# Optimization experiments

Measured on AMD Instinct MI355X. Metric: run time of the kernel, lower is better.

## Reference

```python
import jax, jax.numpy as jnp
import numpy as np

D_MODEL = 2560
NUM_HEADS = 32
NUM_KV_HEADS = 8
HEAD_DIM = 128
ROPE_THETA = 5e6
EPS = 1e-6
G = NUM_KV_HEADS
Q_PER_KV = NUM_HEADS // NUM_KV_HEADS


def setup_inputs() -> dict:
    key = jax.random.key(0)
    ks = jax.random.split(key, 5)
    B, S = 1, 2048
    scale = 0.02
    return {
        "x": jax.random.normal(ks[0], (B, S, D_MODEL), jnp.float32),
        "Wq": jax.random.normal(ks[1], (NUM_HEADS * HEAD_DIM, D_MODEL), jnp.float32) * scale,
        "Wk": jax.random.normal(ks[2], (NUM_KV_HEADS * HEAD_DIM, D_MODEL), jnp.float32) * scale,
        "Wv": jax.random.normal(ks[3], (NUM_KV_HEADS * HEAD_DIM, D_MODEL), jnp.float32) * scale,
        "Wo": jax.random.normal(ks[4], (D_MODEL, NUM_HEADS * HEAD_DIM), jnp.float32) * scale,
        "q_norm_w": jnp.ones((HEAD_DIM,), jnp.float32),
        "k_norm_w": jnp.ones((HEAD_DIM,), jnp.float32),
    }


def _rms_norm(x, w):
    var = jnp.mean(jnp.square(x), axis=-1, keepdims=True)
    return x * jax.lax.rsqrt(var + EPS) * w


def _rope(x, pos):
    # x: (b, h, s, d); HF-style rotate_half RoPE
    d = x.shape[-1]
    inv_freq = 1.0 / (ROPE_THETA ** (jnp.arange(0, d, 2, dtype=jnp.float32) / d))
    ang = pos[:, None].astype(jnp.float32) * inv_freq[None, :]      # (s, d/2)
    cos = jnp.concatenate([jnp.cos(ang), jnp.cos(ang)], axis=-1)     # (s, d)
    sin = jnp.concatenate([jnp.sin(ang), jnp.sin(ang)], axis=-1)
    x1, x2 = x[..., : d // 2], x[..., d // 2 :]
    rot = jnp.concatenate([-x2, x1], axis=-1)
    return x * cos + rot * sin


def reference(x, Wq, Wk, Wv, Wo, q_norm_w, k_norm_w):
    B, S, _ = x.shape
    pos = jnp.arange(S)
    q = (x @ Wq.T).reshape(B, S, NUM_HEADS, HEAD_DIM).transpose(0, 2, 1, 3)
    k = (x @ Wk.T).reshape(B, S, NUM_KV_HEADS, HEAD_DIM).transpose(0, 2, 1, 3)
    v = (x @ Wv.T).reshape(B, S, NUM_KV_HEADS, HEAD_DIM).transpose(0, 2, 1, 3)
    q = _rope(_rms_norm(q, q_norm_w), pos)
    k = _rope(_rms_norm(k, k_norm_w), pos)
    new_cache_k, new_cache_v = k, v
    # GQA: (b, g, h, s, d) against (b, g, k, d)
    qg = q.reshape(B, G, Q_PER_KV, S, HEAD_DIM)
    scores = jnp.einsum("bghsd,bgkd->bghsk", qg, k) / (HEAD_DIM ** 0.5)
    causal = jnp.triu(jnp.full((S, S), -jnp.inf, jnp.float32), k=1)
    scores = scores + causal
    attn = jax.nn.softmax(scores, axis=-1)
    out = jnp.einsum("bghsk,bgkd->bghsd", attn, v)
    out = out.reshape(B, NUM_HEADS, S, HEAD_DIM).transpose(0, 2, 1, 3).reshape(B, S, NUM_HEADS * HEAD_DIM)
    out = out @ Wo.T
    return (out, new_cache_k, new_cache_v)
```

## Files before the change

kernel.cpp:

```cpp
#include <hip/hip_runtime.h>
#include <hip/hip_bf16.h>
#include <math.h>

#define S_LEN  2048
#define DMODEL 2560
#define NHEADS 32
#define NKV    8
#define HD     128
#define QKDIM  (NHEADS * HD)
#define KVDIM  (NKV * HD)

typedef __bf16 bf16x8 __attribute__((ext_vector_type(8)));
typedef float  f32x4  __attribute__((ext_vector_type(4)));
typedef unsigned short u16;

#define AS1 __attribute__((address_space(1)))
#define AS3 __attribute__((address_space(3)))

__device__ __forceinline__ void load16_to_lds(const void* g, void* l) {
    __builtin_amdgcn_global_load_lds((const AS1 void*)g, (AS3 void*)l, 16, 0, 0);
}

__device__ __forceinline__ u16 f2bf(float f) {
    unsigned u = __builtin_bit_cast(unsigned, f);
    return (u16)((u + 0x7fff + ((u >> 16) & 1)) >> 16);
}

#define PHASE_BAR() do { __builtin_amdgcn_sched_barrier(0);            \
                         __builtin_amdgcn_s_barrier();                 \
                         __builtin_amdgcn_sched_barrier(0); } while (0)
#define WAIT_LGKM0() do { asm volatile("s_waitcnt lgkmcnt(0)" ::: "memory"); \
                          __builtin_amdgcn_sched_barrier(0); } while (0)

__device__ __forceinline__ const bf16x8* fragp(const __bf16* hbase, int row, int colb) {
    int b = (row << 7) | colb;
    b ^= ((b >> 7) & 7) << 4;
    return (const bf16x8*)((const char*)hbase + b);
}

__device__ __forceinline__ void stage_half(const __bf16* __restrict__ g0, int Kp,
                                           __bf16* l0, int wave, int lane) {
#pragma unroll
    for (int j = 0; j < 2; ++j) {
        const int p = ((wave * 2 + j) << 10) | (lane << 4);
        const int b = p ^ (((p >> 7) & 7) << 4);
        load16_to_lds((const char*)g0 + (size_t)(b >> 7) * (Kp * 2) + (b & 127),
                      (char*)l0 + ((wave * 2 + j) << 10));
    }
}

#define N4_X   (S_LEN * DMODEL / 4)
#define N4_WQ  (QKDIM * DMODEL / 4)
#define N4_WK  (KVDIM * DMODEL / 4)
#define N4_ALL (N4_X + N4_WQ + 2 * N4_WK)

__global__ __launch_bounds__(256) void convert_inputs(const float* __restrict__ x,
                                                      const float* __restrict__ wq,
                                                      const float* __restrict__ wk,
                                                      const float* __restrict__ wv,
                                                      u16* __restrict__ xb,
                                                      u16* __restrict__ wb) {
    const int stride = gridDim.x * 256;
    for (int i = blockIdx.x * 256 + threadIdx.x; i < N4_ALL; i += stride) {
        const float4* src;
        ushort4* dst;
        if (i < N4_X) {
            src = (const float4*)x + i;
            dst = (ushort4*)xb + i;
        } else {
            const int j = i - N4_X;
            dst = (ushort4*)wb + j;
            if (j < N4_WQ)                  src = (const float4*)wq + j;
            else if (j < N4_WQ + N4_WK)     src = (const float4*)wk + (j - N4_WQ);
            else                            src = (const float4*)wv + (j - N4_WQ - N4_WK);
        }
        float4 v = *src;
        ushort4 r;
        r.x = f2bf(v.x); r.y = f2bf(v.y); r.z = f2bf(v.z); r.w = f2bf(v.w);
        *dst = r;
    }
}

#define N4_OUT (S_LEN * DMODEL / 4)
#define N4_WO  (DMODEL * QKDIM / 4)

__global__ __launch_bounds__(256) void prep_outproj(const float* __restrict__ wo,
                                                    u16* __restrict__ wob,
                                                    float* __restrict__ outz) {
    const int stride = gridDim.x * 256;
    for (int i = blockIdx.x * 256 + threadIdx.x; i < N4_OUT + N4_WO; i += stride) {
        if (i < N4_OUT) {
            ((float4*)outz)[i] = (float4){0.f, 0.f, 0.f, 0.f};
        } else {
            const int j = i - N4_OUT;
            float4 v = ((const float4*)wo)[j];
            ushort4 r;
            r.x = f2bf(v.x); r.y = f2bf(v.y); r.z = f2bf(v.z); r.w = f2bf(v.w);
            ((ushort4*)wob)[j] = r;
        }
    }
}

__global__ __launch_bounds__(64) void rope_table(float* __restrict__ ct,
                                                 float* __restrict__ st) {
    const int s = blockIdx.x;
    const int i = threadIdx.x;
    const double invf = pow(5.0e6, -(double)i / 64.0);
    const double ang  = (double)s * invf;
    ct[s * 64 + i] = (float)cos(ang);
    st[s * 64 + i] = (float)sin(ang);
}

__global__ __launch_bounds__(512, 2) void gemm_qkv_8ph(const __bf16* __restrict__ A,
                                                       const __bf16* __restrict__ Bq,
                                                       const __bf16* __restrict__ Bkv,
                                                       const float* __restrict__ ct,
                                                       const float* __restrict__ st,
                                                       const float* __restrict__ qw,
                                                       const float* __restrict__ kw,
                                                       u16*   __restrict__ qrb,
                                                       float* __restrict__ kc,
                                                       u16*   __restrict__ kcb,
                                                       float* __restrict__ vc,
                                                       u16*   __restrict__ vtb) {
    __shared__ __align__(16) __bf16 Als[4][128 * 64];
    __shared__ __align__(16) __bf16 Bls[4][128 * 64];

    const int K   = DMODEL;
    const int nkt = K / 64;
    const int n0g = blockIdx.x * 256;
    const __bf16* B;
    int n0;
    if (n0g < QKDIM) { B = Bq;  n0 = n0g; }
    else             { B = Bkv; n0 = n0g - QKDIM; }
    const int m0 = blockIdx.y * 256;

    const int tid  = threadIdx.x;
    const int lane = tid & 63;
    const int wave = tid >> 6;
    const int wm   = wave >> 1;
    const int wn   = wave & 1;
    const int frow = lane & 15;
    const int fkq  = lane >> 4;
    const int ha   = wm >> 1;
    const int ar0  = (wm & 1) * 64 + frow;

    f32x4 acc[4][8];
#pragma unroll
    for (int t = 0; t < 4; ++t)
#pragma unroll
        for (int u = 0; u < 8; ++u)
            acc[t][u] = (f32x4){0.f, 0.f, 0.f, 0.f};

    stage_half(A + (size_t)m0 * K,               K, Als[0], wave, lane);
    stage_half(A + (size_t)(m0 + 128) * K,       K, Als[1], wave, lane);
    stage_half(B + (size_t)n0 * K,               K, Bls[0], wave, lane);
    stage_half(B + (size_t)(n0 + 128) * K,       K, Bls[1], wave, lane);
    stage_half(A + (size_t)m0 * K + 64,          K, Als[2], wave, lane);
    stage_half(B + (size_t)n0 * K + 64,          K, Bls[2], wave, lane);
    stage_half(B + (size_t)(n0 + 128) * K + 64,  K, Bls[3], wave, lane);
    asm volatile("s_waitcnt vmcnt(6)" ::: "memory");
    PHASE_BAR();

    for (int kt = 0; kt < nkt; ++kt) {
        const int bf = kt & 1;
        const __bf16* Ahb = Als[bf * 2 + ha];
        const __bf16* Bhb = Bls[bf * 2 + wn];

        bf16x8 a0[2][2], b0[4][2];
#pragma unroll
        for (int mt = 0; mt < 2; ++mt)
#pragma unroll
            for (int kh = 0; kh < 2; ++kh)
                a0[mt][kh] = *fragp(Ahb, ar0 + mt * 16, kh * 64 + fkq * 16);
#pragma unroll
        for (int nt = 0; nt < 4; ++nt)
#pragma unroll
            for (int kh = 0; kh < 2; ++kh)
                b0[nt][kh] = *fragp(Bhb, nt * 16 + frow, kh * 64 + fkq * 16);
        if (kt + 1 < nkt)
            stage_half(A + (size_t)(m0 + 128) * K + (kt + 1) * 64, K,
                       Als[(bf ^ 1) * 2 + 1], wave, lane);
        asm volatile("s_waitcnt lgkmcnt(8)" ::: "memory");
        PHASE_BAR();
        WAIT_LGKM0();
        __builtin_amdgcn_s_setprio(1);
#pragma unroll
        for (int mt = 0; mt < 2; ++mt)
#pragma unroll
            for (int nt = 0; nt < 4; ++nt)
#pragma unroll
                for (int kh = 0; kh < 2; ++kh)
                    acc[mt][nt] = __builtin_amdgcn_mfma_f32_16x16x32_bf16(
                                      a0[mt][kh], b0[nt][kh], acc[mt][nt], 0, 0, 0);
        __builtin_amdgcn_s_setprio(0);
        PHASE_BAR();

        bf16x8 a1[2][2];
#pragma unroll
        for (int mt = 0; mt < 2; ++mt)
#pragma unroll
            for (int kh = 0; kh < 2; ++kh)
                a1[mt][kh] = *fragp(Ahb, ar0 + 32 + mt * 16, kh * 64 + fkq * 16);
        PHASE_BAR();
        WAIT_LGKM0();
        __builtin_amdgcn_s_setprio(1);
#pragma unroll
        for (int mt = 0; mt < 2; ++mt)
#pragma unroll
            for (int nt = 0; nt < 4; ++nt)
#pragma unroll
                for (int kh = 0; kh < 2; ++kh)
                    acc[2 + mt][nt] = __builtin_amdgcn_mfma_f32_16x16x32_bf16(
                                          a1[mt][kh], b0[nt][kh], acc[2 + mt][nt], 0, 0, 0);
        __builtin_amdgcn_s_setprio(0);
        PHASE_BAR();

        bf16x8 b1[4][2];
#pragma unroll
        for (int nt = 0; nt < 4; ++nt)
#pragma unroll
            for (int kh = 0; kh < 2; ++kh)
                b1[nt][kh] = *fragp(Bhb, (4 + nt) * 16 + frow, kh * 64 + fkq * 16);
        if (kt + 2 < nkt)
            stage_half(A + (size_t)m0 * K + (kt + 2) * 64, K,
                       Als[bf * 2 + 0], wave, lane);
        PHASE_BAR();
        WAIT_LGKM0();
        __builtin_amdgcn_s_setprio(1);
#pragma unroll
        for (int mt = 0; mt < 2; ++mt)
#pragma unroll
            for (int nt = 0; nt < 4; ++nt)
#pragma unroll
                for (int kh = 0; kh < 2; ++kh)
                    acc[2 + mt][4 + nt] = __builtin_amdgcn_mfma_f32_16x16x32_bf16(
                                              a1[mt][kh], b1[nt][kh], acc[2 + mt][4 + nt], 0, 0, 0);
        __builtin_amdgcn_s_setprio(0);
        PHASE_BAR();

        if (kt + 2 < nkt) {
            stage_half(B + (size_t)n0 * K + (kt + 2) * 64,         K,
                       Bls[bf * 2 + 0], wave, lane);
            stage_half(B + (size_t)(n0 + 128) * K + (kt + 2) * 64, K,
                       Bls[bf * 2 + 1], wave, lane);
        }
        PHASE_BAR();
        WAIT_LGKM0();
        __builtin_amdgcn_s_setprio(1);
#pragma unroll
        for (int mt = 0; mt < 2; ++mt)
#pragma unroll
            for (int nt = 0; nt < 4; ++nt)
#pragma unroll
                for (int kh = 0; kh < 2; ++kh)
                    acc[mt][4 + nt] = __builtin_amdgcn_mfma_f32_16x16x32_bf16(
                                          a0[mt][kh], b1[nt][kh], acc[mt][4 + nt], 0, 0, 0);
        __builtin_amdgcn_s_setprio(0);
        if (kt < nkt - 2) asm volatile("s_waitcnt vmcnt(6)" ::: "memory");
        else              asm volatile("s_waitcnt vmcnt(0)" ::: "memory");
        PHASE_BAR();
    }

    const int fr = frow;
    const int fq = fkq;
    const int nw = n0g + wn * 128;
    if (n0g < QKDIM + KVDIM) {
        const int isQ = (n0g < QKDIM) ? 1 : 0;
        const float* w = isQ ? qw : kw;
        float wv[8];
#pragma unroll
        for (int u = 0; u < 8; ++u) wv[u] = w[u * 16 + fr];

#pragma unroll
        for (int mt = 0; mt < 4; ++mt) {
#pragma unroll
            for (int r = 0; r < 4; ++r) {
                float ss = 0.f;
#pragma unroll
                for (int u = 0; u < 8; ++u) ss += acc[mt][u][r] * acc[mt][u][r];
                ss += __shfl_xor(ss, 1);
                ss += __shfl_xor(ss, 2);
                ss += __shfl_xor(ss, 4);
                ss += __shfl_xor(ss, 8);
                const float rstd = rsqrtf(ss * (1.0f / 128.0f) + 1e-6f);
                const int s = m0 + wm * 64 + mt * 16 + fq * 4 + r;
#pragma unroll
                for (int u = 0; u < 4; ++u) {
                    const float cs  = ct[s * 64 + u * 16 + fr];
                    const float sn  = st[s * 64 + u * 16 + fr];
                    const float ylo = acc[mt][u][r]     * rstd * wv[u];
                    const float yhi = acc[mt][u + 4][r] * rstd * wv[u + 4];
                    const float olo = ylo * cs - yhi * sn;
                    const float ohi = yhi * cs + ylo * sn;
                    if (isQ) {
                        const int h = nw >> 7;
                        const size_t base = ((size_t)h * S_LEN + s) * HD;
                        qrb[base + u * 16 + fr]       = f2bf(olo * 0.12751743f);
                        qrb[base + (u + 4) * 16 + fr] = f2bf(ohi * 0.12751743f);
                    } else {
                        const int g = (nw - QKDIM) >> 7;
                        const size_t base = ((size_t)g * S_LEN + s) * HD;
                        kc [base + u * 16 + fr]       = olo;
                        kc [base + (u + 4) * 16 + fr] = ohi;
                        kcb[base + u * 16 + fr]       = f2bf(olo);
                        kcb[base + (u + 4) * 16 + fr] = f2bf(ohi);
                    }
                }
            }
        }
    } else {
        const int g = (nw - QKDIM - KVDIM) >> 7;
#pragma unroll
        for (int mt = 0; mt < 4; ++mt) {
            const int sb = m0 + wm * 64 + mt * 16 + fq * 4;
#pragma unroll
            for (int u = 0; u < 8; ++u) {
                const int d = u * 16 + fr;
                ushort4 o;
                o.x = f2bf(acc[mt][u][0]); o.y = f2bf(acc[mt][u][1]);
                o.z = f2bf(acc[mt][u][2]); o.w = f2bf(acc[mt][u][3]);
                *(ushort4*)&vtb[((size_t)g * HD + d) * S_LEN + sb] = o;
#pragma unroll
                for (int r = 0; r < 4; ++r)
                    vc[((size_t)g * S_LEN + sb + r) * HD + d] = acc[mt][u][r];
            }
        }
    }
}

__global__ __launch_bounds__(512, 2) void gemm_out_8ph(const __bf16* __restrict__ A,
                                                       const __bf16* __restrict__ B,
                                                       float* __restrict__ C) {
    __shared__ __align__(16) __bf16 Als[4][128 * 64];
    __shared__ __align__(16) __bf16 Bls[4][128 * 64];

    const int K   = QKDIM;
    const int z   = blockIdx.z;
    const int ks0 = (z == 0) ? 0 : 22 + (z - 1) * 21;
    const int L   = (z == 0) ? 22 : 21;
    const int ko0 = ks0 * 64;
    const int n0  = blockIdx.x * 256;
    const int m0  = blockIdx.y * 256;

    const int tid  = threadIdx.x;
    const int lane = tid & 63;
    const int wave = tid >> 6;
    const int wm   = wave >> 1;
    const int wn   = wave & 1;
    const int frow = lane & 15;
    const int fkq  = lane >> 4;
    const int ha   = wm >> 1;
    const int ar0  = (wm & 1) * 64 + frow;

    f32x4 acc[4][8];
#pragma unroll
    for (int t = 0; t < 4; ++t)
#pragma unroll
        for (int u = 0; u < 8; ++u)
            acc[t][u] = (f32x4){0.f, 0.f, 0.f, 0.f};

    stage_half(A + (size_t)m0 * K + ko0,              K, Als[0], wave, lane);
    stage_half(A + (size_t)(m0 + 128) * K + ko0,      K, Als[1], wave, lane);
    stage_half(B + (size_t)n0 * K + ko0,              K, Bls[0], wave, lane);
    stage_half(B + (size_t)(n0 + 128) * K + ko0,      K, Bls[1], wave, lane);
    stage_half(A + (size_t)m0 * K + ko0 + 64,         K, Als[2], wave, lane);
    stage_half(B + (size_t)n0 * K + ko0 + 64,         K, Bls[2], wave, lane);
    stage_half(B + (size_t)(n0 + 128) * K + ko0 + 64, K, Bls[3], wave, lane);
    asm volatile("s_waitcnt vmcnt(6)" ::: "memory");
    PHASE_BAR();

    for (int j = 0; j < L; ++j) {
        const int bf = j & 1;
        const __bf16* Ahb = Als[bf * 2 + ha];
        const __bf16* Bhb = Bls[bf * 2 + wn];

        bf16x8 a0[2][2], b0[4][2];
#pragma unroll
        for (int mt = 0; mt < 2; ++mt)
#pragma unroll
            for (int kh = 0; kh < 2; ++kh)
                a0[mt][kh] = *fragp(Ahb, ar0 + mt * 16, kh * 64 + fkq * 16);
#pragma unroll
        for (int nt = 0; nt < 4; ++nt)
#pragma unroll
            for (int kh = 0; kh < 2; ++kh)
                b0[nt][kh] = *fragp(Bhb, nt * 16 + frow, kh * 64 + fkq * 16);
        if (j + 1 < L)
            stage_half(A + (size_t)(m0 + 128) * K + ko0 + (j + 1) * 64, K,
                       Als[(bf ^ 1) * 2 + 1], wave, lane);
        asm volatile("s_waitcnt lgkmcnt(8)" ::: "memory");
        PHASE_BAR();
        WAIT_LGKM0();
        __builtin_amdgcn_s_setprio(1);
#pragma unroll
        for (int mt = 0; mt < 2; ++mt)
#pragma unroll
            for (int nt = 0; nt < 4; ++nt)
#pragma unroll
                for (int kh = 0; kh < 2; ++kh)
                    acc[mt][nt] = __builtin_amdgcn_mfma_f32_16x16x32_bf16(
                                      a0[mt][kh], b0[nt][kh], acc[mt][nt], 0, 0, 0);
        __builtin_amdgcn_s_setprio(0);
        PHASE_BAR();

        bf16x8 a1[2][2];
#pragma unroll
        for (int mt = 0; mt < 2; ++mt)
#pragma unroll
            for (int kh = 0; kh < 2; ++kh)
                a1[mt][kh] = *fragp(Ahb, ar0 + 32 + mt * 16, kh * 64 + fkq * 16);
        PHASE_BAR();
        WAIT_LGKM0();
        __builtin_amdgcn_s_setprio(1);
#pragma unroll
        for (int mt = 0; mt < 2; ++mt)
#pragma unroll
            for (int nt = 0; nt < 4; ++nt)
#pragma unroll
                for (int kh = 0; kh < 2; ++kh)
                    acc[2 + mt][nt] = __builtin_amdgcn_mfma_f32_16x16x32_bf16(
                                          a1[mt][kh], b0[nt][kh], acc[2 + mt][nt], 0, 0, 0);
        __builtin_amdgcn_s_setprio(0);
        PHASE_BAR();

        bf16x8 b1[4][2];
#pragma unroll
        for (int nt = 0; nt < 4; ++nt)
#pragma unroll
            for (int kh = 0; kh < 2; ++kh)
                b1[nt][kh] = *fragp(Bhb, (4 + nt) * 16 + frow, kh * 64 + fkq * 16);
        if (j + 2 < L)
            stage_half(A + (size_t)m0 * K + ko0 + (j + 2) * 64, K,
                       Als[bf * 2 + 0], wave, lane);
        PHASE_BAR();
        WAIT_LGKM0();
        __builtin_amdgcn_s_setprio(1);
#pragma unroll
        for (int mt = 0; mt < 2; ++mt)
#pragma unroll
            for (int nt = 0; nt < 4; ++nt)
#pragma unroll
                for (int kh = 0; kh < 2; ++kh)
                    acc[2 + mt][4 + nt] = __builtin_amdgcn_mfma_f32_16x16x32_bf16(
                                              a1[mt][kh], b1[nt][kh], acc[2 + mt][4 + nt], 0, 0, 0);
        __builtin_amdgcn_s_setprio(0);
        PHASE_BAR();

        if (j + 2 < L) {
            stage_half(B + (size_t)n0 * K + ko0 + (j + 2) * 64,         K,
                       Bls[bf * 2 + 0], wave, lane);
            stage_half(B + (size_t)(n0 + 128) * K + ko0 + (j + 2) * 64, K,
                       Bls[bf * 2 + 1], wave, lane);
        }
        PHASE_BAR();
        WAIT_LGKM0();
        __builtin_amdgcn_s_setprio(1);
#pragma unroll
        for (int mt = 0; mt < 2; ++mt)
#pragma unroll
            for (int nt = 0; nt < 4; ++nt)
#pragma unroll
                for (int kh = 0; kh < 2; ++kh)
                    acc[mt][4 + nt] = __builtin_amdgcn_mfma_f32_16x16x32_bf16(
                                          a0[mt][kh], b1[nt][kh], acc[mt][4 + nt], 0, 0, 0);
        __builtin_amdgcn_s_setprio(0);
        if (j < L - 2) asm volatile("s_waitcnt vmcnt(6)" ::: "memory");
        else           asm volatile("s_waitcnt vmcnt(0)" ::: "memory");
        PHASE_BAR();
    }

#pragma unroll
    for (int mt = 0; mt < 4; ++mt) {
#pragma unroll
        for (int r = 0; r < 4; ++r) {
            const int s = m0 + wm * 64 + mt * 16 + fkq * 4 + r;
            float* crow = C + (size_t)s * DMODEL + n0 + wn * 128 + frow;
#pragma unroll
            for (int u = 0; u < 8; ++u)
                unsafeAtomicAdd(crow + u * 16, acc[mt][u][r]);
        }
    }
}

__device__ __forceinline__ void attn_tile_swapped(
        const bf16x8 aq[4], f32x4 o_acc[8], float& m_i, float& l_i,
        const __bf16* __restrict__ Kl, const __bf16* __restrict__ Vl,
        int lane, int fr, int fq, int qm, int kbase, bool diag) {
    f32x4 sT[4];
#pragma unroll
    for (int u = 0; u < 4; ++u) sT[u] = (f32x4){0.f, 0.f, 0.f, 0.f};
    __builtin_amdgcn_s_setprio(1);
#pragma unroll
    for (int u = 0; u < 4; ++u)
#pragma unroll
        for (int ks = 0; ks < 4; ++ks)
            sT[u] = __builtin_amdgcn_mfma_f32_16x16x32_bf16(
                        *(const bf16x8*)&Kl[((u * 4 + ks) * 64 + lane) * 8],
                        aq[ks], sT[u], 0, 0, 0);
    __builtin_amdgcn_s_setprio(0);

    if (diag) {
#pragma unroll
        for (int u = 0; u < 4; ++u)
#pragma unroll
            for (int r = 0; r < 4; ++r)
                if (kbase + u * 16 + fq * 4 + r > qm + fr)
                    sT[u][r] = -INFINITY;
    }

    float mx = sT[0][0];
#pragma unroll
    for (int u = 0; u < 4; ++u)
#pragma unroll
        for (int r = 0; r < 4; ++r) mx = fmaxf(mx, sT[u][r]);
    mx = fmaxf(mx, __shfl_xor(mx, 16));
    mx = fmaxf(mx, __shfl_xor(mx, 32));

    if (__any(mx > m_i + 8.0f)) {
        const float m_new = fmaxf(m_i, mx);
        const float alpha = exp2f(m_i - m_new);
        m_i = m_new;
        l_i *= alpha;
#pragma unroll
        for (int r = 0; r < 4; ++r) {
            const float a = __shfl(alpha, fq * 4 + r);
#pragma unroll
            for (int dt = 0; dt < 8; ++dt) o_acc[dt][r] *= a;
        }
    }

    float p[4][4];
    float ps = 0.f;
#pragma unroll
    for (int u = 0; u < 4; ++u)
#pragma unroll
        for (int r = 0; r < 4; ++r) {
            p[u][r] = exp2f(sT[u][r] - m_i);
            ps += p[u][r];
        }
    ps += __shfl_xor(ps, 16);
    ps += __shfl_xor(ps, 32);
    l_i += ps;

    unsigned pk[4][2];
#pragma unroll
    for (int u = 0; u < 4; ++u)
#pragma unroll
        for (int hh = 0; hh < 2; ++hh)
            asm("v_cvt_pk_bf16_f32 %0, %1, %2"
                : "=v"(pk[u][hh]) : "v"(p[u][2 * hh]), "v"(p[u][2 * hh + 1]));

    const int slA = fr + 16 * ((fq & 1) * 2);
    const int slB = slA + 16;
    bf16x8 ap[2];
#pragma unroll
    for (int ks = 0; ks < 2; ++ks) {
        unsigned w[4];
#pragma unroll
        for (int jp = 0; jp < 4; ++jp) {
            const int sl = (jp & 2) ? slB : slA;
            const unsigned v0 = (unsigned)__shfl((int)pk[2 * ks + 0][jp & 1], sl);
            const unsigned v1 = (unsigned)__shfl((int)pk[2 * ks + 1][jp & 1], sl);
            w[jp] = (fq & 2) ? v1 : v0;
        }
        ap[ks] = __builtin_bit_cast(bf16x8, (uint4){w[0], w[1], w[2], w[3]});
    }

    __builtin_amdgcn_s_setprio(1);
#pragma unroll
    for (int dt = 0; dt < 8; ++dt)
#pragma unroll
        for (int ks = 0; ks < 2; ++ks)
            o_acc[dt] = __builtin_amdgcn_mfma_f32_16x16x32_bf16(
                            ap[ks],
                            *(const bf16x8*)&Vl[((dt * 2 + ks) * 64 + lane) * 8],
                            o_acc[dt], 0, 0, 0);
    __builtin_amdgcn_s_setprio(0);
}

__global__ __launch_bounds__(256, 2) void attn_mfma(const __bf16* __restrict__ Qb,
                                                    const __bf16* __restrict__ Kb,
                                                    const __bf16* __restrict__ Vt,
                                                    u16* __restrict__ Ob) {
    __shared__ __align__(16) __bf16 Kls[2][16 * 64 * 8];
    __shared__ __align__(16) __bf16 Vls[2][16 * 64 * 8];

    const int h    = blockIdx.x;
    const int g    = h >> 2;
    const int pair = blockIdx.y;
    const int ytl  = pair;
    const int yth  = (S_LEN / 64 - 1) - pair;
    const int q0l  = ytl * 64;
    const int q0h  = yth * 64;
    const int tid  = threadIdx.x;
    const int lane = tid & 63;
    const int wave = tid >> 6;
    const int fr   = lane & 15;
    const int fq   = lane >> 4;

    {
        const __bf16* Qh = Qb + ((size_t)h * S_LEN + q0h + wave * 16 + fr) * HD;
        const __bf16* Ql = Qb + ((size_t)h * S_LEN + q0l + wave * 16 + fr) * HD;
#pragma unroll
        for (int ks = 0; ks < 4; ++ks) {
            load16_to_lds(Qh + ks * 32 + fq * 8, &Kls[0][(size_t)((wave * 4 + ks) * 64) * 8]);
            load16_to_lds(Ql + ks * 32 + fq * 8, &Kls[1][(size_t)((wave * 4 + ks) * 64) * 8]);
        }
    }
    __syncthreads();
    bf16x8 aqh[4], aql[4];
#pragma unroll
    for (int ks = 0; ks < 4; ++ks) {
        aqh[ks] = *(const bf16x8*)&Kls[0][((wave * 4 + ks) * 64 + lane) * 8];
        aql[ks] = *(const bf16x8*)&Kls[1][((wave * 4 + ks) * 64 + lane) * 8];
    }
    __syncthreads();

    float m_h = -INFINITY, l_h = 0.f, m_l = -INFINITY, l_l = 0.f;
    f32x4 o_h[8], o_l[8];
#pragma unroll
    for (int dt = 0; dt < 8; ++dt) {
        o_h[dt] = (f32x4){0.f, 0.f, 0.f, 0.f};
        o_l[dt] = (f32x4){0.f, 0.f, 0.f, 0.f};
    }

    {
        const __bf16* Kg = Kb + ((size_t)g * S_LEN + wave * 16 + fr) * HD;
#pragma unroll
        for (int ks = 0; ks < 4; ++ks)
            load16_to_lds(Kg + ks * 32 + fq * 8, &Kls[0][(size_t)((wave * 4 + ks) * 64) * 8]);
#pragma unroll
        for (int i = 0; i < 2; ++i) {
            const int dt = wave * 2 + i;
            const __bf16* Vg = Vt + ((size_t)g * HD + dt * 16 + fr) * S_LEN;
#pragma unroll
            for (int ks = 0; ks < 2; ++ks)
                load16_to_lds(Vg + ks * 32 + fq * 8, &Vls[0][(size_t)((dt * 2 + ks) * 64) * 8]);
        }
    }
    __syncthreads();

    for (int kt = 0; kt <= yth; ++kt) {
        const int buf = kt & 1;
        if (kt < yth) {
            const int nb = buf ^ 1;
            const __bf16* Kg = Kb + ((size_t)g * S_LEN + (kt + 1) * 64 + wave * 16 + fr) * HD;
#pragma unroll
            for (int ks = 0; ks < 4; ++ks)
                load16_to_lds(Kg + ks * 32 + fq * 8, &Kls[nb][(size_t)((wave * 4 + ks) * 64) * 8]);
#pragma unroll
            for (int i = 0; i < 2; ++i) {
                const int dt = wave * 2 + i;
                const __bf16* Vg = Vt + ((size_t)g * HD + dt * 16 + fr) * S_LEN + (kt + 1) * 64;
#pragma unroll
                for (int ks = 0; ks < 2; ++ks)
                    load16_to_lds(Vg + ks * 32 + fq * 8, &Vls[nb][(size_t)((dt * 2 + ks) * 64) * 8]);
            }
        }

        attn_tile_swapped(aqh, o_h, m_h, l_h, Kls[buf], Vls[buf],
                          lane, fr, fq, q0h + wave * 16, kt * 64, kt == yth);
        if (kt <= ytl)
            attn_tile_swapped(aql, o_l, m_l, l_l, Kls[buf], Vls[buf],
                              lane, fr, fq, q0l + wave * 16, kt * 64, kt == ytl);

        __syncthreads();
    }

#pragma unroll
    for (int r = 0; r < 4; ++r) {
        const float ih = 1.0f / __shfl(l_h, fq * 4 + r);
        const float il = 1.0f / __shfl(l_l, fq * 4 + r);
        const int sh = q0h + wave * 16 + fq * 4 + r;
        const int sl = q0l + wave * 16 + fq * 4 + r;
#pragma unroll
        for (int dt = 0; dt < 8; ++dt) {
            Ob[(size_t)sh * QKDIM + h * HD + dt * 16 + fr] = f2bf(o_h[dt][r] * ih);
            Ob[(size_t)sl * QKDIM + h * HD + dt * 16 + fr] = f2bf(o_l[dt][r] * il);
        }
    }
}

extern "C" void kernel_launch(void* const* d_in, const int* in_sizes, int n_in,
                              void* d_out, int out_size, void* d_ws, size_t ws_size,
                              hipStream_t stream) {
    const float* x  = (const float*)d_in[0];
    const float* Wq = (const float*)d_in[1];
    const float* Wk = (const float*)d_in[2];
    const float* Wv = (const float*)d_in[3];
    const float* Wo = (const float*)d_in[4];
    const float* qw = (const float*)d_in[5];
    const float* kw = (const float*)d_in[6];

    float* out     = (float*)d_out;
    float* cache_k = out + (size_t)S_LEN * DMODEL;
    float* cache_v = cache_k + (size_t)NKV * S_LEN * HD;

    u16* wsu = (u16*)d_ws;
    u16* qrb = wsu;
    u16* kcb = qrb + (size_t)NHEADS * S_LEN * HD;
    u16* vtb = kcb + (size_t)NKV * S_LEN * HD;
    u16* Wqb = vtb + (size_t)NKV * S_LEN * HD;
    u16* Wkb = Wqb + (size_t)QKDIM * DMODEL;
    u16* aob = Wqb;
    u16* Wob = aob + (size_t)S_LEN * QKDIM;
    float* ct = (float*)(Wqb + (size_t)S_LEN * QKDIM + (size_t)DMODEL * QKDIM);
    float* st = ct + S_LEN * 64;
    u16* xb  = (u16*)out;

    convert_inputs<<<4096, 256, 0, stream>>>(x, Wq, Wk, Wv, xb, Wqb);
    rope_table<<<S_LEN, 64, 0, stream>>>(ct, st);

    gemm_qkv_8ph<<<dim3((QKDIM + 2 * KVDIM) / 256, S_LEN / 256), 512, 0, stream>>>(
        (const __bf16*)xb, (const __bf16*)Wqb, (const __bf16*)Wkb,
        ct, st, qw, kw, qrb, cache_k, kcb, cache_v, vtb);

    prep_outproj<<<2048, 256, 0, stream>>>(Wo, Wob, out);
    attn_mfma<<<dim3(NHEADS, S_LEN / 128), 256, 0, stream>>>(
        (const __bf16*)qrb, (const __bf16*)kcb, (const __bf16*)vtb, aob);

    gemm_out_8ph<<<dim3(DMODEL / 256, S_LEN / 256, 3), 512, 0, stream>>>(
        (const __bf16*)aob, (const __bf16*)Wob, out);
}
```

Baseline: 422.7 us.

## Replace paired causal q-tiles with one tile per block and single-buffer K

The attention kernel stops pairing a low and a high query tile in each block. It now launches one 64-row query tile per block, doubling the grid, with the heaviest tiles scheduled first. K goes from double buffering to a single buffer that is reloaded after the QK MFMAs behind a phase barrier, while V stays double-buffered. Launch bounds rise to 3 blocks per CU to exploit the lower register and LDS use. The aim is more occupancy and finer-grained load balance, at the cost of reloading Q and K per block and exposing more K-load latency.

Measured after the change: 416.1 us. No clear change (-1.6%).

```diff
diff --git a/kernel.cpp b/kernel.cpp
--- a/kernel.cpp
+++ b/kernel.cpp
@@ -483,153 +483,47 @@
     }
 }
 
-__device__ __forceinline__ void attn_tile_swapped(
-        const bf16x8 aq[4], f32x4 o_acc[8], float& m_i, float& l_i,
-        const __bf16* __restrict__ Kl, const __bf16* __restrict__ Vl,
-        int lane, int fr, int fq, int qm, int kbase, bool diag) {
-    f32x4 sT[4];
-#pragma unroll
-    for (int u = 0; u < 4; ++u) sT[u] = (f32x4){0.f, 0.f, 0.f, 0.f};
-    __builtin_amdgcn_s_setprio(1);
-#pragma unroll
-    for (int u = 0; u < 4; ++u)
-#pragma unroll
-        for (int ks = 0; ks < 4; ++ks)
-            sT[u] = __builtin_amdgcn_mfma_f32_16x16x32_bf16(
-                        *(const bf16x8*)&Kl[((u * 4 + ks) * 64 + lane) * 8],
-                        aq[ks], sT[u], 0, 0, 0);
-    __builtin_amdgcn_s_setprio(0);
-
-    if (diag) {
-#pragma unroll
-        for (int u = 0; u < 4; ++u)
-#pragma unroll
-            for (int r = 0; r < 4; ++r)
-                if (kbase + u * 16 + fq * 4 + r > qm + fr)
-                    sT[u][r] = -INFINITY;
-    }
-
-    float mx = sT[0][0];
-#pragma unroll
-    for (int u = 0; u < 4; ++u)
-#pragma unroll
-        for (int r = 0; r < 4; ++r) mx = fmaxf(mx, sT[u][r]);
-    mx = fmaxf(mx, __shfl_xor(mx, 16));
-    mx = fmaxf(mx, __shfl_xor(mx, 32));
-
-    if (__any(mx > m_i + 8.0f)) {
-        const float m_new = fmaxf(m_i, mx);
-        const float alpha = exp2f(m_i - m_new);
-        m_i = m_new;
-        l_i *= alpha;
-#pragma unroll
-        for (int r = 0; r < 4; ++r) {
-            const float a = __shfl(alpha, fq * 4 + r);
-#pragma unroll
-            for (int dt = 0; dt < 8; ++dt) o_acc[dt][r] *= a;
-        }
-    }
-
-    float p[4][4];
-    float ps = 0.f;
-#pragma unroll
-    for (int u = 0; u < 4; ++u)
-#pragma unroll
-        for (int r = 0; r < 4; ++r) {
-            p[u][r] = exp2f(sT[u][r] - m_i);
-            ps += p[u][r];
-        }
-    ps += __shfl_xor(ps, 16);
-    ps += __shfl_xor(ps, 32);
-    l_i += ps;
-
-    unsigned pk[4][2];
-#pragma unroll
-    for (int u = 0; u < 4; ++u)
-#pragma unroll
-        for (int hh = 0; hh < 2; ++hh)
-            asm("v_cvt_pk_bf16_f32 %0, %1, %2"
-                : "=v"(pk[u][hh]) : "v"(p[u][2 * hh]), "v"(p[u][2 * hh + 1]));
-
-    const int slA = fr + 16 * ((fq & 1) * 2);
-    const int slB = slA + 16;
-    bf16x8 ap[2];
-#pragma unroll
-    for (int ks = 0; ks < 2; ++ks) {
-        unsigned w[4];
-#pragma unroll
-        for (int jp = 0; jp < 4; ++jp) {
-            const int sl = (jp & 2) ? slB : slA;
-            const unsigned v0 = (unsigned)__shfl((int)pk[2 * ks + 0][jp & 1], sl);
-            const unsigned v1 = (unsigned)__shfl((int)pk[2 * ks + 1][jp & 1], sl);
-            w[jp] = (fq & 2) ? v1 : v0;
-        }
-        ap[ks] = __builtin_bit_cast(bf16x8, (uint4){w[0], w[1], w[2], w[3]});
-    }
-
-    __builtin_amdgcn_s_setprio(1);
-#pragma unroll
-    for (int dt = 0; dt < 8; ++dt)
-#pragma unroll
-        for (int ks = 0; ks < 2; ++ks)
-            o_acc[dt] = __builtin_amdgcn_mfma_f32_16x16x32_bf16(
-                            ap[ks],
-                            *(const bf16x8*)&Vl[((dt * 2 + ks) * 64 + lane) * 8],
-                            o_acc[dt], 0, 0, 0);
-    __builtin_amdgcn_s_setprio(0);
-}
-
-__global__ __launch_bounds__(256, 2) void attn_mfma(const __bf16* __restrict__ Qb,
+__global__ __launch_bounds__(256, 3) void attn_mfma(const __bf16* __restrict__ Qb,
                                                     const __bf16* __restrict__ Kb,
                                                     const __bf16* __restrict__ Vt,
                                                     u16* __restrict__ Ob) {
-    __shared__ __align__(16) __bf16 Kls[2][16 * 64 * 8];
+    __shared__ __align__(16) __bf16 Kls[16 * 64 * 8];
     __shared__ __align__(16) __bf16 Vls[2][16 * 64 * 8];
 
     const int h    = blockIdx.x;
     const int g    = h >> 2;
-    const int pair = blockIdx.y;
-    const int ytl  = pair;
-    const int yth  = (S_LEN / 64 - 1) - pair;
-    const int q0l  = ytl * 64;
-    const int q0h  = yth * 64;
+    const int yt   = (S_LEN / 64 - 1) - blockIdx.y;
+    const int q0   = yt * 64;
     const int tid  = threadIdx.x;
     const int lane = tid & 63;
     const int wave = tid >> 6;
     const int fr   = lane & 15;
     const int fq   = lane >> 4;
+    const int qm   = q0 + wave * 16;
 
     {
-        const __bf16* Qh = Qb + ((size_t)h * S_LEN + q0h + wave * 16 + fr) * HD;
-        const __bf16* Ql = Qb + ((size_t)h * S_LEN + q0l + wave * 16 + fr) * HD;
-#pragma unroll
-        for (int ks = 0; ks < 4; ++ks) {
-            load16_to_lds(Qh + ks * 32 + fq * 8, &Kls[0][(size_t)((wave * 4 + ks) * 64) * 8]);
-            load16_to_lds(Ql + ks * 32 + fq * 8, &Kls[1][(size_t)((wave * 4 + ks) * 64) * 8]);
-        }
+        const __bf16* Qg = Qb + ((size_t)h * S_LEN + q0 + wave * 16 + fr) * HD;
+#pragma unroll
+        for (int ks = 0; ks < 4; ++ks)
+            load16_to_lds(Qg + ks * 32 + fq * 8, &Vls[0][(size_t)((wave * 4 + ks) * 64) * 8]);
     }
     __syncthreads();
-    bf16x8 aqh[4], aql[4];
-#pragma unroll
-    for (int ks = 0; ks < 4; ++ks) {
-        aqh[ks] = *(const bf16x8*)&Kls[0][((wave * 4 + ks) * 64 + lane) * 8];
-        aql[ks] = *(const bf16x8*)&Kls[1][((wave * 4 + ks) * 64 + lane) * 8];
-    }
+    bf16x8 aq[4];
+#pragma unroll
+    for (int ks = 0; ks < 4; ++ks)
+        aq[ks] = *(const bf16x8*)&Vls[0][((wave * 4 + ks) * 64 + lane) * 8];
     __syncthreads();
 
-    float m_h = -INFINITY, l_h = 0.f, m_l = -INFINITY, l_l = 0.f;
-    f32x4 o_h[8], o_l[8];
-#pragma unroll
-    for (int dt = 0; dt < 8; ++dt) {
-        o_h[dt] = (f32x4){0.f, 0.f, 0.f, 0.f};
-        o_l[dt] = (f32x4){0.f, 0.f, 0.f, 0.f};
-    }
+    float m_i = -INFINITY, l_i = 0.f;
+    f32x4 o_acc[8];
+#pragma unroll
+    for (int dt = 0; dt < 8; ++dt) o_acc[dt] = (f32x4){0.f, 0.f, 0.f, 0.f};
 
     {
         const __bf16* Kg = Kb + ((size_t)g * S_LEN + wave * 16 + fr) * HD;
 #pragma unroll
         for (int ks = 0; ks < 4; ++ks)
-            load16_to_lds(Kg + ks * 32 + fq * 8, &Kls[0][(size_t)((wave * 4 + ks) * 64) * 8]);
+            load16_to_lds(Kg + ks * 32 + fq * 8, &Kls[(size_t)((wave * 4 + ks) * 64) * 8]);
 #pragma unroll
         for (int i = 0; i < 2; ++i) {
             const int dt = wave * 2 + i;
@@ -641,44 +535,130 @@
     }
     __syncthreads();
 
-    for (int kt = 0; kt <= yth; ++kt) {
-        const int buf = kt & 1;
-        if (kt < yth) {
-            const int nb = buf ^ 1;
-            const __bf16* Kg = Kb + ((size_t)g * S_LEN + (kt + 1) * 64 + wave * 16 + fr) * HD;
-#pragma unroll
-            for (int ks = 0; ks < 4; ++ks)
-                load16_to_lds(Kg + ks * 32 + fq * 8, &Kls[nb][(size_t)((wave * 4 + ks) * 64) * 8]);
+    for (int kt = 0; kt <= yt; ++kt) {
+        const int vb = kt & 1;
+
+        if (kt < yt) {
 #pragma unroll
             for (int i = 0; i < 2; ++i) {
                 const int dt = wave * 2 + i;
                 const __bf16* Vg = Vt + ((size_t)g * HD + dt * 16 + fr) * S_LEN + (kt + 1) * 64;
 #pragma unroll
                 for (int ks = 0; ks < 2; ++ks)
-                    load16_to_lds(Vg + ks * 32 + fq * 8, &Vls[nb][(size_t)((dt * 2 + ks) * 64) * 8]);
+                    load16_to_lds(Vg + ks * 32 + fq * 8,
+                                  &Vls[vb ^ 1][(size_t)((dt * 2 + ks) * 64) * 8]);
             }
         }
 
-        attn_tile_swapped(aqh, o_h, m_h, l_h, Kls[buf], Vls[buf],
-                          lane, fr, fq, q0h + wave * 16, kt * 64, kt == yth);
-        if (kt <= ytl)
-            attn_tile_swapped(aql, o_l, m_l, l_l, Kls[buf], Vls[buf],
-                              lane, fr, fq, q0l + wave * 16, kt * 64, kt == ytl);
+        f32x4 sT[4];
+#pragma unroll
+        for (int u = 0; u < 4; ++u) sT[u] = (f32x4){0.f, 0.f, 0.f, 0.f};
+        __builtin_amdgcn_s_setprio(1);
+#pragma unroll
+        for (int u = 0; u < 4; ++u)
+#pragma unroll
+            for (int ks = 0; ks < 4; ++ks)
+                sT[u] = __builtin_amdgcn_mfma_f32_16x16x32_bf16(
+                            *(const bf16x8*)&Kls[((u * 4 + ks) * 64 + lane) * 8],
+                            aq[ks], sT[u], 0, 0, 0);
+        __builtin_amdgcn_s_setprio(0);
+
+        PHASE_BAR();
+        if (kt < yt) {
+            const __bf16* Kg = Kb + ((size_t)g * S_LEN + (kt + 1) * 64 + wave * 16 + fr) * HD;
+#pragma unroll
+            for (int ks = 0; ks < 4; ++ks)
+                load16_to_lds(Kg + ks * 32 + fq * 8, &Kls[(size_t)((wave * 4 + ks) * 64) * 8]);
+        }
+
+        if (kt == yt) {
+#pragma unroll
+            for (int u = 0; u < 4; ++u)
+#pragma unroll
+                for (int r = 0; r < 4; ++r)
+                    if (kt * 64 + u * 16 + fq * 4 + r > qm + fr)
+                        sT[u][r] = -INFINITY;
+        }
+
+        float mx = sT[0][0];
+#pragma unroll
+        for (int u = 0; u < 4; ++u)
+#pragma unroll
+            for (int r = 0; r < 4; ++r) mx = fmaxf(mx, sT[u][r]);
+        mx = fmaxf(mx, __shfl_xor(mx, 16));
+        mx = fmaxf(mx, __shfl_xor(mx, 32));
+
+        if (__any(mx > m_i + 8.0f)) {
+            const float m_new = fmaxf(m_i, mx);
+            const float alpha = exp2f(m_i - m_new);
+            m_i = m_new;
+            l_i *= alpha;
+#pragma unroll
+            for (int r = 0; r < 4; ++r) {
+                const float a = __shfl(alpha, fq * 4 + r);
+#pragma unroll
+                for (int dt = 0; dt < 8; ++dt) o_acc[dt][r] *= a;
+            }
+        }
+
+        float p[4][4];
+        float ps = 0.f;
+#pragma unroll
+        for (int u = 0; u < 4; ++u)
+#pragma unroll
+            for (int r = 0; r < 4; ++r) {
+                p[u][r] = exp2f(sT[u][r] - m_i);
+                ps += p[u][r];
+            }
+        ps += __shfl_xor(ps, 16);
+        ps += __shfl_xor(ps, 32);
+        l_i += ps;
+
+        unsigned pk[4][2];
+#pragma unroll
+        for (int u = 0; u < 4; ++u)
+#pragma unroll
+            for (int hh = 0; hh < 2; ++hh)
+                asm("v_cvt_pk_bf16_f32 %0, %1, %2"
+                    : "=v"(pk[u][hh]) : "v"(p[u][2 * hh]), "v"(p[u][2 * hh + 1]));
+
+        const int slA = fr + 16 * ((fq & 1) * 2);
+        const int slB = slA + 16;
+        bf16x8 ap[2];
+#pragma unroll
+        for (int ks = 0; ks < 2; ++ks) {
+            unsigned w[4];
+#pragma unroll
+            for (int jp = 0; jp < 4; ++jp) {
+                const int sl = (jp & 2) ? slB : slA;
+                const unsigned v0 = (unsigned)__shfl((int)pk[2 * ks + 0][jp & 1], sl);
+                const unsigned v1 = (unsigned)__shfl((int)pk[2 * ks + 1][jp & 1], sl);
+                w[jp] = (fq & 2) ? v1 : v0;
+            }
+            ap[ks] = __builtin_bit_cast(bf16x8, (uint4){w[0], w[1], w[2], w[3]});
+        }
+
+        __builtin_amdgcn_s_setprio(1);
+#pragma unroll
+        for (int dt = 0; dt < 8; ++dt)
+#pragma unroll
+            for (int ks = 0; ks < 2; ++ks)
+                o_acc[dt] = __builtin_amdgcn_mfma_f32_16x16x32_bf16(
+                                ap[ks],
+                                *(const bf16x8*)&Vls[vb][((dt * 2 + ks) * 64 + lane) * 8],
+                                o_acc[dt], 0, 0, 0);
+        __builtin_amdgcn_s_setprio(0);
 
         __syncthreads();
     }
 
 #pragma unroll
     for (int r = 0; r < 4; ++r) {
-        const float ih = 1.0f / __shfl(l_h, fq * 4 + r);
-        const float il = 1.0f / __shfl(l_l, fq * 4 + r);
-        const int sh = q0h + wave * 16 + fq * 4 + r;
-        const int sl = q0l + wave * 16 + fq * 4 + r;
-#pragma unroll
-        for (int dt = 0; dt < 8; ++dt) {
-            Ob[(size_t)sh * QKDIM + h * HD + dt * 16 + fr] = f2bf(o_h[dt][r] * ih);
-            Ob[(size_t)sl * QKDIM + h * HD + dt * 16 + fr] = f2bf(o_l[dt][r] * il);
-        }
+        const float inv_l = 1.0f / __shfl(l_i, fq * 4 + r);
+        const int s = q0 + wave * 16 + fq * 4 + r;
+#pragma unroll
+        for (int dt = 0; dt < 8; ++dt)
+            Ob[(size_t)s * QKDIM + h * HD + dt * 16 + fr] = f2bf(o_acc[dt][r] * inv_l);
     }
 }
 
@@ -717,7 +697,7 @@
         ct, st, qw, kw, qrb, cache_k, kcb, cache_v, vtb);
 
     prep_outproj<<<2048, 256, 0, stream>>>(Wo, Wob, out);
-    attn_mfma<<<dim3(NHEADS, S_LEN / 128), 256, 0, stream>>>(
+    attn_mfma<<<dim3(NHEADS, S_LEN / 64), 256, 0, stream>>>(
         (const __bf16*)qrb, (const __bf16*)kcb, (const __bf16*)vtb, aob);
 
     gemm_out_8ph<<<dim3(DMODEL / 256, S_LEN / 256, 3), 512, 0, stream>>>(
```
